# Performance work log

Measured on AMD Instinct MI355X. Metric: run time of the kernel, lower is better.

Reference implementation:

```python
import jax, jax.numpy as jnp
import numpy as np

VOCAB, EMB, HID, LAYERS, SEQ, BATCH = 10000, 1024, 1024, 2, 64, 64


def setup_inputs() -> dict:
    key = jax.random.key(0)
    ks = jax.random.split(key, 12)
    b = 1.0 / np.sqrt(HID)
    u = lambda k, shape, bd: jax.random.uniform(k, shape, jnp.float32, -bd, bd)
    return {
        "inputs": jax.random.randint(ks[0], (SEQ, BATCH), 0, VOCAB),
        "hidden": jnp.zeros((LAYERS, BATCH, HID), jnp.float32),
        "emb": u(ks[1], (VOCAB, EMB), 0.1),
        "W0": u(ks[2], (EMB, 3 * HID), b),
        "U0": u(ks[3], (HID, 3 * HID), b),
        "bw0": u(ks[4], (3 * HID,), b),
        "bu0": u(ks[5], (3 * HID,), b),
        "W1": u(ks[6], (HID, 3 * HID), b),
        "U1": u(ks[7], (HID, 3 * HID), b),
        "bw1": u(ks[8], (3 * HID,), b),
        "bu1": u(ks[9], (3 * HID,), b),
        "fcW": u(ks[10], (VOCAB, HID), 0.1),
        "fcb": jnp.zeros((VOCAB,), jnp.float32),
    }


def gru_cell(x, h, W, U, bw, bu):
    gx = x @ W + bw            # [B, 3H]
    gh = h @ U + bu            # [B, 3H]
    i_r, i_z, i_n = jnp.split(gx, 3, axis=1)
    h_r, h_z, h_n = jnp.split(gh, 3, axis=1)
    r = jax.nn.sigmoid(i_r + h_r)
    z = jax.nn.sigmoid(i_z + h_z)
    h_tilde = jnp.tanh(i_n + r * h_n)
    return (1.0 - z) * h + z * h_tilde


def reference(inputs, hidden, emb, W0, U0, bw0, bu0, W1, U1, bw1, bu1, fcW, fcb):
    # dp_keep_prob = 1.0 -> dropout is identity (eval-mode reference)
    def step(hid, tok):
        x = emb[tok]                                   # [B, EMB]
        h0 = gru_cell(x, hid[0], W0, U0, bw0, bu0)     # [B, H]
        h1 = gru_cell(h0, hid[1], W1, U1, bw1, bu1)    # [B, H]
        y = h1 @ fcW.T + fcb                           # [B, V]
        return jnp.stack([h0, h1]), y

    hidden_f, logits = jax.lax.scan(step, hidden, inputs)
    return logits, hidden_f
```

## Files before the change

### kernel.cpp

```cpp
#include <hip/hip_runtime.h>
#include <math.h>

#define SEQL 64
#define BATCHN 64
#define HID 1024
#define EMBD 1024
#define VOCAB 10000
#define G3 3072
#define NPAD 10240
#define AROWS 4096
#define HSLOT 65536

typedef float f4v __attribute__((ext_vector_type(4)));
typedef unsigned short us4 __attribute__((ext_vector_type(4)));
typedef unsigned short us8 __attribute__((ext_vector_type(8)));
typedef __bf16 bf8v __attribute__((ext_vector_type(8)));

__device__ __forceinline__ unsigned short f2bf(float f) {
    unsigned u = __float_as_uint(f);
    u += 0x7fffu + ((u >> 16) & 1u);
    return (unsigned short)(u >> 16);
}
__device__ __forceinline__ float bf2f(unsigned short h) {
    return __uint_as_float(((unsigned)h) << 16);
}
__device__ __forceinline__ void split2(float f, unsigned short &hi, unsigned short &lo) {
    hi = f2bf(f);
    lo = f2bf(f - bf2f(hi));
}
__device__ __forceinline__ f4v mfma16(us8 a, us8 b, f4v c) {
    return __builtin_amdgcn_mfma_f32_16x16x32_bf16(
        __builtin_bit_cast(bf8v, a), __builtin_bit_cast(bf8v, b), c, 0, 0, 0);
}
__device__ __forceinline__ float sigmoidf_(float x) { return 1.f / (1.f + expf(-x)); }

__device__ __forceinline__ size_t htile_off(int b, int j) {
    return ((size_t)((((b >> 4) * 32 + (j >> 5)) * 64) + ((j >> 3) & 3) * 16 + (b & 15))) * 8 + (j & 7);
}

__global__ __launch_bounds__(256)
void tile_weights_kernel(const float* __restrict__ U0, const float* __restrict__ W1,
                         const float* __restrict__ U1, const float* __restrict__ W0,
                         unsigned short* __restrict__ hi, unsigned short* __restrict__ lo)
{
    __shared__ float tile[32][65];
    const int mat = blockIdx.z;
    const float* src = (mat == 0) ? U0 : (mat == 1) ? W1 : (mat == 2) ? U1 : W0;
    const int n0 = blockIdx.x * 64, k0 = blockIdx.y * 32;
    const int t = threadIdx.x, tx = t & 63, ty = t >> 6;
#pragma unroll
    for (int s = 0; s < 8; s++)
        tile[ty * 8 + s][tx] = src[(size_t)(k0 + ty * 8 + s) * G3 + n0 + tx];
    __syncthreads();
    const int c = t >> 6, lane = t & 63, fr = lane & 15, kg = lane >> 4;
    const int cc = (n0 >> 4) + c;
    const size_t off = (((size_t)(mat * 192 + cc) * 32 + (k0 >> 5)) * 64 + lane) * 8;
    us8 h8, l8;
#pragma unroll
    for (int e = 0; e < 8; e++) {
        unsigned short a, b;
        split2(tile[kg * 8 + e][c * 16 + fr], a, b);
        h8[e] = a; l8[e] = b;
    }
    *(us8*)(hi + off) = h8;
    *(us8*)(lo + off) = l8;
}

__global__ __launch_bounds__(256)
void tile_fc_kernel(const float* __restrict__ fcW,
                    unsigned short* __restrict__ hi, unsigned short* __restrict__ lo)
{
    const int cc = blockIdx.x;
    const int tid = threadIdx.x;
#pragma unroll
    for (int q = 0; q < 8; q++) {
        const int o = tid * 8 + q;
        const int ks = o >> 6, lane = o & 63;
        const int fr = lane & 15, kg = lane >> 4;
        const int row = cc * 16 + fr;
        const int col = ks * 32 + kg * 8;
        us8 h8, l8;
        if (row < VOCAB) {
            f4v v0 = *(const f4v*)(fcW + (size_t)row * HID + col);
            f4v v1 = *(const f4v*)(fcW + (size_t)row * HID + col + 4);
#pragma unroll
            for (int e = 0; e < 4; e++) {
                unsigned short a, b;
                split2(v0[e], a, b); h8[e] = a; l8[e] = b;
                split2(v1[e], a, b); h8[4 + e] = a; l8[4 + e] = b;
            }
        } else {
            h8 = (us8){0,0,0,0,0,0,0,0};
            l8 = (us8){0,0,0,0,0,0,0,0};
        }
        const size_t off = (((size_t)cc * 32 + ks) * 64 + lane) * 8;
        *(us8*)(hi + off) = h8;
        *(us8*)(lo + off) = l8;
    }
}

__global__ void fcb_pad_kernel(const float* __restrict__ fcb, float* __restrict__ fcb_pad)
{
    int idx = blockIdx.x * 256 + threadIdx.x;
    if (idx < NPAD) fcb_pad[idx] = (idx < VOCAB) ? fcb[idx] : 0.f;
}

__global__ void small_prep_kernel(const float* __restrict__ hidden,
                                  unsigned short* __restrict__ h0th, unsigned short* __restrict__ h0tl,
                                  unsigned short* __restrict__ h1th, unsigned short* __restrict__ h1tl)
{
    int idx = blockIdx.x * 256 + threadIdx.x;
    if (idx < BATCHN * HID) {
        int b = idx >> 10, j = idx & 1023;
        size_t o = htile_off(b, j);
        unsigned short a1, b1;
        split2(hidden[idx], a1, b1);                 h0th[o] = a1; h0tl[o] = b1;
        split2(hidden[BATCHN * HID + idx], a1, b1);  h1th[o] = a1; h1tl[o] = b1;
    }
}

__global__ __launch_bounds__(256)
void gx0_gemm_kernel(const int* __restrict__ tok, const float* __restrict__ emb,
                     const unsigned short* __restrict__ Wthi, const unsigned short* __restrict__ Wtlo,
                     float* __restrict__ C)
{
    __shared__ unsigned short Ah[128][40], Al[128][40];
    const int bswz = blockIdx.x;
    const int xcd = bswz & 7, s = bswz >> 3;
    const int col0 = (xcd + 8 * (s >> 5)) * 128;
    const int row0 = (s & 31) * 128;
    const int tid = threadIdx.x;
    const int lane = tid & 63, wave = tid >> 6;
    const int wm = wave >> 1, wn = wave & 1;
    const int srow = tid >> 1;
    const int shalf = (tid & 1) * 16;

    const float* asrc = emb + (size_t)tok[row0 + srow] * EMBD + shalf;
    const int fr = lane & 15, fk = (lane >> 4) * 8;
    const int cc0 = (col0 >> 4) + wn * 4;

    f4v a[4];
#pragma unroll
    for (int q = 0; q < 4; q++) a[q] = *(const f4v*)(asrc + q * 4);

    f4v acc[4][4] = {};
    for (int k0 = 0; k0 < EMBD; k0 += 32) {
        __syncthreads();
        us8 ahv[2], alv[2];
#pragma unroll
        for (int q = 0; q < 4; q++)
#pragma unroll
            for (int j = 0; j < 4; j++) {
                unsigned short h, l;
                split2(a[q][j], h, l);
                ahv[q >> 1][(q & 1) * 4 + j] = h;
                alv[q >> 1][(q & 1) * 4 + j] = l;
            }
        *(us8*)(&Ah[srow][shalf]) = ahv[0];     *(us8*)(&Ah[srow][shalf + 8]) = ahv[1];
        *(us8*)(&Al[srow][shalf]) = alv[0];     *(us8*)(&Al[srow][shalf + 8]) = alv[1];
        __syncthreads();
        if (k0 + 32 < EMBD) {
#pragma unroll
            for (int q = 0; q < 4; q++) a[q] = *(const f4v*)(asrc + k0 + 32 + q * 4);
        }
        const int ks = k0 >> 5;
        us8 bfh[4], bfl[4];
#pragma unroll
        for (int n = 0; n < 4; n++) {
            const size_t bo = (((size_t)(3 * 192 + cc0 + n) * 32 + ks) * 64 + lane) * 8;
            bfh[n] = *(const us8*)(Wthi + bo);
            bfl[n] = *(const us8*)(Wtlo + bo);
        }
        us8 afh[4], afl[4];
#pragma unroll
        for (int m = 0; m < 4; m++) {
            afh[m] = *(const us8*)(&Ah[wm * 64 + m * 16 + fr][fk]);
            afl[m] = *(const us8*)(&Al[wm * 64 + m * 16 + fr][fk]);
        }
#pragma unroll
        for (int n = 0; n < 4; n++)
#pragma unroll
            for (int m = 0; m < 4; m++) {
                acc[m][n] = mfma16(afh[m], bfh[n], acc[m][n]);
                acc[m][n] = mfma16(afh[m], bfl[n], acc[m][n]);
                acc[m][n] = mfma16(afl[m], bfh[n], acc[m][n]);
            }
    }
    const int fq = lane >> 4;
#pragma unroll
    for (int m = 0; m < 4; m++)
#pragma unroll
        for (int n = 0; n < 4; n++)
#pragma unroll
            for (int i = 0; i < 4; i++) {
                int r = row0 + wm * 64 + m * 16 + fq * 4 + i;
                int c = col0 + wn * 64 + n * 16 + fr;
                C[(size_t)r * G3 + c] = acc[m][n][i];
            }
}

__global__ __launch_bounds__(256)
void logits_gemm_kernel(const unsigned short* __restrict__ h1t_hi, const unsigned short* __restrict__ h1t_lo,
                        const unsigned short* __restrict__ Bhi, const unsigned short* __restrict__ Blo,
                        const float* __restrict__ bias, float* __restrict__ C)
{
    const int bswz = blockIdx.x;
    const int xcd = bswz & 7, s = bswz >> 3;
    const int col0 = (xcd + 8 * (s >> 5)) * 128;
    const int row0 = (s & 31) * 128;
    const int t0 = row0 >> 6;
    const int tid = threadIdx.x;
    const int lane = tid & 63, wave = tid >> 6;
    const int wm = wave >> 1, wn = wave & 1;
    const int fr = lane & 15;
    const int cc0 = (col0 >> 4) + wn * 4;

    f4v acc[4][4] = {};
    const size_t abase = ((size_t)(t0 + wm) * 128) * 512 + (size_t)lane * 8;

    for (int ks = 0; ks < 32; ks++) {
        us8 afh[4], afl[4], bfh[4], bfl[4];
#pragma unroll
        for (int m = 0; m < 4; m++) {
            const size_t ao = abase + (size_t)(m * 32 + ks) * 512;
            afh[m] = *(const us8*)(h1t_hi + ao);
            afl[m] = *(const us8*)(h1t_lo + ao);
        }
#pragma unroll
        for (int n = 0; n < 4; n++) {
            const size_t bo = (((size_t)(cc0 + n) * 32 + ks) * 64 + lane) * 8;
            bfh[n] = *(const us8*)(Bhi + bo);
            bfl[n] = *(const us8*)(Blo + bo);
        }
#pragma unroll
        for (int n = 0; n < 4; n++)
#pragma unroll
            for (int m = 0; m < 4; m++) {
                acc[m][n] = mfma16(afh[m], bfh[n], acc[m][n]);
                acc[m][n] = mfma16(afh[m], bfl[n], acc[m][n]);
                acc[m][n] = mfma16(afl[m], bfh[n], acc[m][n]);
            }
    }
    const int fq = lane >> 4;
#pragma unroll
    for (int m = 0; m < 4; m++)
#pragma unroll
        for (int n = 0; n < 4; n++)
#pragma unroll
            for (int i = 0; i < 4; i++) {
                int r = row0 + wm * 64 + m * 16 + fq * 4 + i;
                int c = col0 + wn * 64 + n * 16 + fr;
                float v = acc[m][n][i] + bias[c];
                if (c < VOCAB) C[(size_t)r * VOCAB + c] = v;
            }
}

template <int T0, int T1>
__global__ __launch_bounds__(256)
void step_gemm_kernel(const unsigned short* __restrict__ h0hi, const unsigned short* __restrict__ h0lo,
                      const unsigned short* __restrict__ h1hi, const unsigned short* __restrict__ h1lo,
                      const unsigned short* __restrict__ Wthi, const unsigned short* __restrict__ Wtlo,
                      float* __restrict__ P)
{
    const int tid = threadIdx.x, lane = tid & 63, wave = tid >> 6;
    const int jc = blockIdx.x >> 3, kh = blockIdx.x & 7;
    const int ks = kh * 4 + wave;
    const size_t abase = ((size_t)ks * 64 + lane) * 8;

    f4v acc[9][4] = {};
    us8 ah[4], al[4];

    if (T0 < 6) {
#pragma unroll
        for (int m = 0; m < 4; m++) {
            ah[m] = *(const us8*)(h0hi + abase + (size_t)m * 16384);
            al[m] = *(const us8*)(h0lo + abase + (size_t)m * 16384);
        }
#pragma unroll
        for (int t2 = T0; t2 < ((T1 < 6) ? T1 : 6); ++t2) {
            const int mat = t2 / 3, g = t2 % 3;
            const size_t base = (((size_t)(mat * 192 + g * 64 + jc) * 32 + ks) * 64 + lane) * 8;
            us8 bh = *(const us8*)(Wthi + base);
            us8 bl = *(const us8*)(Wtlo + base);
#pragma unroll
            for (int m = 0; m < 4; ++m) {
                acc[t2][m] = mfma16(ah[m], bh, acc[t2][m]);
                acc[t2][m] = mfma16(ah[m], bl, acc[t2][m]);
                acc[t2][m] = mfma16(al[m], bh, acc[t2][m]);
            }
        }
    }
    if (T1 > 6) {
#pragma unroll
        for (int m = 0; m < 4; m++) {
            ah[m] = *(const us8*)(h1hi + abase + (size_t)m * 16384);
            al[m] = *(const us8*)(h1lo + abase + (size_t)m * 16384);
        }
#pragma unroll
        for (int t2 = 6; t2 < T1; ++t2) {
            const int g = t2 % 3;
            const size_t base = (((size_t)(2 * 192 + g * 64 + jc) * 32 + ks) * 64 + lane) * 8;
            us8 bh = *(const us8*)(Wthi + base);
            us8 bl = *(const us8*)(Wtlo + base);
#pragma unroll
            for (int m = 0; m < 4; ++m) {
                acc[t2][m] = mfma16(ah[m], bh, acc[t2][m]);
                acc[t2][m] = mfma16(ah[m], bl, acc[t2][m]);
                acc[t2][m] = mfma16(al[m], bh, acc[t2][m]);
            }
        }
    }

    __shared__ f4v red[4][2][4][64];
    const int rrow = (lane >> 4) * 4, rcol = lane & 15;
#pragma unroll
    for (int c = 0; c < 5; ++c) {
        const int ta = 2 * c, tb = 2 * c + 1;
        if (tb >= T0 && ta < T1) {
#pragma unroll
            for (int u = 0; u < 2; ++u) {
                const int t2 = 2 * c + u;
                if (t2 >= T0 && t2 < T1) {
#pragma unroll
                    for (int m = 0; m < 4; ++m)
                        red[wave][u][m][lane] = acc[t2][m];
                }
            }
            __syncthreads();
#pragma unroll
            for (int s2 = 0; s2 < 2; ++s2) {
                const int combo = wave * 2 + s2;
                const int u = combo >> 2, m = combo & 3;
                const int t2 = 2 * c + u;
                if (t2 >= T0 && t2 < T1) {
                    f4v v = (red[0][u][m][lane] + red[1][u][m][lane])
                          + (red[2][u][m][lane] + red[3][u][m][lane]);
#pragma unroll
                    for (int i = 0; i < 4; ++i)
                        P[(((size_t)kh * 9 + t2) * 64 + (m * 16 + rrow + i)) * 1024 + jc * 16 + rcol]
                            = v[i];
                }
            }
            __syncthreads();
        }
    }
}

template <int T0, int T1>
__global__ __launch_bounds__(256)
void step_reduce_kernel(const float* __restrict__ P, const float* __restrict__ gx0next,
                        const float* __restrict__ bw0, const float* __restrict__ bu0,
                        const float* __restrict__ bw1, const float* __restrict__ bu1,
                        const unsigned short* __restrict__ h0hi, const unsigned short* __restrict__ h0lo,
                        const unsigned short* __restrict__ h1hi, const unsigned short* __restrict__ h1lo,
                        unsigned short* __restrict__ h0o_hi, unsigned short* __restrict__ h0o_lo,
                        unsigned short* __restrict__ h1o_hi, unsigned short* __restrict__ h1o_lo)
{
    const int idx = blockIdx.x * 256 + threadIdx.x;
    const int b = idx >> 10, j = idx & 1023;
    float G[9];
#pragma unroll
    for (int t2 = T0; t2 < T1; t2++) {
        const float* p = P + ((size_t)t2 * 64 + b) * 1024 + j;
        float s0 = 0.f, s1 = 0.f;
#pragma unroll
        for (int kh = 0; kh < 4; kh++) {
            s0 += p[(size_t)(kh * 9) * 64 * 1024];
            s1 += p[(size_t)((kh + 4) * 9) * 64 * 1024];
        }
        G[t2] = s0 + s1;
    }
    const size_t po = htile_off(b, j);
    if (T0 == 0) {
        float sr  = gx0next[(size_t)b * G3 + j]            + bw0[j]           + G[0] + bu0[j];
        float sz  = gx0next[(size_t)b * G3 + HID + j]      + bw0[HID + j]     + G[1] + bu0[HID + j];
        float gxn = gx0next[(size_t)b * G3 + 2 * HID + j]  + bw0[2 * HID + j];
        float ghn = G[2] + bu0[2 * HID + j];
        float r = sigmoidf_(sr);
        float z = sigmoidf_(sz);
        float ht = tanhf(gxn + r * ghn);
        float hp = bf2f(h0hi[po]) + bf2f(h0lo[po]);
        float hn = (1.f - z) * hp + z * ht;
        unsigned short hh, hl2; split2(hn, hh, hl2);
        h0o_hi[po] = hh; h0o_lo[po] = hl2;
    }
    if (T1 > 3) {
        float sr  = G[3] + bw1[j]           + G[6] + bu1[j];
        float sz  = G[4] + bw1[HID + j]     + G[7] + bu1[HID + j];
        float gxn = G[5] + bw1[2 * HID + j];
        float ghn = G[8] + bu1[2 * HID + j];
        float r = sigmoidf_(sr);
        float z = sigmoidf_(sz);
        float ht = tanhf(gxn + r * ghn);
        float hp = bf2f(h1hi[po]) + bf2f(h1lo[po]);
        float hn = (1.f - z) * hp + z * ht;
        unsigned short hh, hl2; split2(hn, hh, hl2);
        h1o_hi[po] = hh; h1o_lo[po] = hl2;
    }
}

__global__ void hidden_out_kernel(const unsigned short* __restrict__ h0hi, const unsigned short* __restrict__ h0lo,
                                  const unsigned short* __restrict__ h1hi, const unsigned short* __restrict__ h1lo,
                                  float* __restrict__ out)
{
    int i = blockIdx.x * 256 + threadIdx.x;
    if (i < BATCHN * HID) {
        int b = i >> 10, j = i & 1023;
        size_t o = htile_off(b, j);
        out[i] = bf2f(h0hi[o]) + bf2f(h0lo[o]);
        out[BATCHN * HID + i] = bf2f(h1hi[o]) + bf2f(h1lo[o]);
    }
}

extern "C" void kernel_launch(void* const* d_in, const int* in_sizes, int n_in,
                              void* d_out, int out_size, void* d_ws, size_t ws_size,
                              hipStream_t stream)
{
    (void)in_sizes; (void)n_in; (void)out_size;
    const int*   tok    = (const int*)  d_in[0];
    const float* hidden = (const float*)d_in[1];
    const float* emb    = (const float*)d_in[2];
    const float* W0     = (const float*)d_in[3];
    const float* U0     = (const float*)d_in[4];
    const float* bw0    = (const float*)d_in[5];
    const float* bu0    = (const float*)d_in[6];
    const float* W1     = (const float*)d_in[7];
    const float* U1     = (const float*)d_in[8];
    const float* bw1    = (const float*)d_in[9];
    const float* bu1    = (const float*)d_in[10];
    const float* fcW    = (const float*)d_in[11];
    const float* fcb    = (const float*)d_in[12];
    float* out = (float*)d_out;

    char* wsp = (char*)d_ws;
    size_t used = 0;
    auto alloc = [&](size_t bytes) -> char* {
        char* p = wsp + used;
        used += (bytes + 255) & ~(size_t)255;
        return p;
    };
    unsigned short* Wt_hi = (unsigned short*)alloc((size_t)4 * G3 * HID * 2);
    unsigned short* Wt_lo = (unsigned short*)alloc((size_t)4 * G3 * HID * 2);
    float*          GX0   = (float*)alloc((size_t)AROWS * G3 * 4);
    unsigned short* H0Thi = (unsigned short*)alloc((size_t)SEQL * HSLOT * 2);
    unsigned short* H0Tlo = (unsigned short*)alloc((size_t)SEQL * HSLOT * 2);
    unsigned short* H1Thi = (unsigned short*)alloc((size_t)SEQL * HSLOT * 2);
    unsigned short* H1Tlo = (unsigned short*)alloc((size_t)SEQL * HSLOT * 2);
    float*          P     = (float*)alloc((size_t)8 * 9 * BATCHN * HID * 4);
    unsigned short* h0ith = (unsigned short*)alloc((size_t)HSLOT * 2);
    unsigned short* h0itl = (unsigned short*)alloc((size_t)HSLOT * 2);
    unsigned short* h1ith = (unsigned short*)alloc((size_t)HSLOT * 2);
    unsigned short* h1itl = (unsigned short*)alloc((size_t)HSLOT * 2);
    if (used > ws_size) return;

    unsigned short* fcWhi = Wt_hi;
    unsigned short* fcWlo = Wt_lo;
    float*          fcbp  = (float*)((char*)Wt_hi + (size_t)NPAD * HID * 2);

    tile_weights_kernel<<<dim3(48, 32, 4), 256, 0, stream>>>(U0, W1, U1, W0, Wt_hi, Wt_lo);
    small_prep_kernel<<<256, 256, 0, stream>>>(hidden, h0ith, h0itl, h1ith, h1itl);
    gx0_gemm_kernel<<<768, 256, 0, stream>>>(tok, emb, Wt_hi, Wt_lo, GX0);

    step_gemm_kernel<0, 3><<<512, 256, 0, stream>>>(
        h0ith, h0itl, h1ith, h1itl, Wt_hi, Wt_lo, P);
    step_reduce_kernel<0, 3><<<256, 256, 0, stream>>>(
        P, GX0, bw0, bu0, bw1, bu1,
        h0ith, h0itl, h1ith, h1itl,
        H0Thi, H0Tlo,
        H1Thi + (size_t)63 * HSLOT, H1Tlo + (size_t)63 * HSLOT);

    for (int t = 0; t < 63; t++) {
        const unsigned short* h0h = H0Thi + (size_t)t * HSLOT;
        const unsigned short* h0l = H0Tlo + (size_t)t * HSLOT;
        const unsigned short* a1h = (t == 0) ? h1ith : H1Thi + (size_t)(t - 1) * HSLOT;
        const unsigned short* a1l = (t == 0) ? h1itl : H1Tlo + (size_t)(t - 1) * HSLOT;
        step_gemm_kernel<0, 9><<<512, 256, 0, stream>>>(
            h0h, h0l, a1h, a1l, Wt_hi, Wt_lo, P);
        step_reduce_kernel<0, 9><<<256, 256, 0, stream>>>(
            P, GX0 + (size_t)(t + 1) * BATCHN * G3, bw0, bu0, bw1, bu1,
            h0h, h0l, a1h, a1l,
            H0Thi + (size_t)(t + 1) * HSLOT, H0Tlo + (size_t)(t + 1) * HSLOT,
            H1Thi + (size_t)t * HSLOT, H1Tlo + (size_t)t * HSLOT);
    }
    step_gemm_kernel<3, 9><<<512, 256, 0, stream>>>(
        H0Thi + (size_t)63 * HSLOT, H0Tlo + (size_t)63 * HSLOT,
        H1Thi + (size_t)62 * HSLOT, H1Tlo + (size_t)62 * HSLOT,
        Wt_hi, Wt_lo, P);
    step_reduce_kernel<3, 9><<<256, 256, 0, stream>>>(
        P, GX0, bw0, bu0, bw1, bu1,
        H0Thi + (size_t)63 * HSLOT, H0Tlo + (size_t)63 * HSLOT,
        H1Thi + (size_t)62 * HSLOT, H1Tlo + (size_t)62 * HSLOT,
        h0ith, h0itl,
        H1Thi + (size_t)63 * HSLOT, H1Tlo + (size_t)63 * HSLOT);

    hidden_out_kernel<<<256, 256, 0, stream>>>(
        H0Thi + (size_t)63 * HSLOT, H0Tlo + (size_t)63 * HSLOT,
        H1Thi + (size_t)63 * HSLOT, H1Tlo + (size_t)63 * HSLOT,
        out + (size_t)AROWS * VOCAB);

    tile_fc_kernel<<<NPAD / 16, 256, 0, stream>>>(fcW, fcWhi, fcWlo);
    fcb_pad_kernel<<<(NPAD + 255) / 256, 256, 0, stream>>>(fcb, fcbp);
    logits_gemm_kernel<<<2560, 256, 0, stream>>>(
        H1Thi, H1Tlo, fcWhi, fcWlo, fcbp, out);
}
```

Before: 1.555 ms.

## Stage fcW tiles in LDS for logits GEMM and fuse tail kernels

The logits GEMM now uses 512-thread blocks over 256x128 tiles. The fcW hi/lo slices are staged through padded shared memory with a register prefetch of the next k-slice, so B data is shared across more rows instead of each wave loading pre-tiled fragments from global memory. The fcW split now writes a plain row-major layout in one elementwise kernel that also pads the bias. The hidden-state output copy moves into the final step_reduce kernel. Together these remove two launches and aim to cut global B traffic, at the cost of extra barriers per k-step and shared-memory pressure.

```diff
diff --git a/kernel.cpp b/kernel.cpp
--- a/kernel.cpp
+++ b/kernel.cpp
@@ -66,43 +66,21 @@
     *(us8*)(lo + off) = l8;
 }
 
-__global__ __launch_bounds__(256)
-void tile_fc_kernel(const float* __restrict__ fcW,
-                    unsigned short* __restrict__ hi, unsigned short* __restrict__ lo)
-{
-    const int cc = blockIdx.x;
-    const int tid = threadIdx.x;
-#pragma unroll
-    for (int q = 0; q < 8; q++) {
-        const int o = tid * 8 + q;
-        const int ks = o >> 6, lane = o & 63;
-        const int fr = lane & 15, kg = lane >> 4;
-        const int row = cc * 16 + fr;
-        const int col = ks * 32 + kg * 8;
-        us8 h8, l8;
-        if (row < VOCAB) {
-            f4v v0 = *(const f4v*)(fcW + (size_t)row * HID + col);
-            f4v v1 = *(const f4v*)(fcW + (size_t)row * HID + col + 4);
-#pragma unroll
-            for (int e = 0; e < 4; e++) {
-                unsigned short a, b;
-                split2(v0[e], a, b); h8[e] = a; l8[e] = b;
-                split2(v1[e], a, b); h8[4 + e] = a; l8[4 + e] = b;
-            }
-        } else {
-            h8 = (us8){0,0,0,0,0,0,0,0};
-            l8 = (us8){0,0,0,0,0,0,0,0};
-        }
-        const size_t off = (((size_t)cc * 32 + ks) * 64 + lane) * 8;
-        *(us8*)(hi + off) = h8;
-        *(us8*)(lo + off) = l8;
-    }
-}
-
-__global__ void fcb_pad_kernel(const float* __restrict__ fcb, float* __restrict__ fcb_pad)
-{
-    int idx = blockIdx.x * 256 + threadIdx.x;
-    if (idx < NPAD) fcb_pad[idx] = (idx < VOCAB) ? fcb[idx] : 0.f;
+__global__ void fc_pad_split_kernel(const float* __restrict__ fcW,
+                                    unsigned short* __restrict__ hi, unsigned short* __restrict__ lo,
+                                    const float* __restrict__ fcb, float* __restrict__ fcb_pad)
+{
+    size_t g = (size_t)blockIdx.x * 256 + threadIdx.x;
+    if (g < NPAD) fcb_pad[g] = (g < VOCAB) ? fcb[g] : 0.f;
+    size_t i = g * 4;
+    size_t row = i >> 10;
+    f4v v = {0.f, 0.f, 0.f, 0.f};
+    if (row < VOCAB) v = *(const f4v*)(fcW + i);
+    us4 h, l;
+#pragma unroll
+    for (int j = 0; j < 4; j++) { unsigned short a, b; split2(v[j], a, b); h[j] = a; l[j] = b; }
+    *(us4*)(hi + i) = h;
+    *(us4*)(lo + i) = l;
 }
 
 __global__ void small_prep_kernel(const float* __restrict__ hidden,
@@ -199,27 +177,45 @@
             }
 }
 
-__global__ __launch_bounds__(256)
+__global__ __launch_bounds__(512)
 void logits_gemm_kernel(const unsigned short* __restrict__ h1t_hi, const unsigned short* __restrict__ h1t_lo,
                         const unsigned short* __restrict__ Bhi, const unsigned short* __restrict__ Blo,
                         const float* __restrict__ bias, float* __restrict__ C)
 {
+    __shared__ unsigned short Bh[128][40], Bl[128][40];
     const int bswz = blockIdx.x;
     const int xcd = bswz & 7, s = bswz >> 3;
-    const int col0 = (xcd + 8 * (s >> 5)) * 128;
-    const int row0 = (s & 31) * 128;
+    const int rt = xcd + 8 * (s / 80);
+    const int col0 = (s % 80) * 128;
+    const int row0 = rt * 256;
     const int t0 = row0 >> 6;
     const int tid = threadIdx.x;
     const int lane = tid & 63, wave = tid >> 6;
     const int wm = wave >> 1, wn = wave & 1;
-    const int fr = lane & 15;
-    const int cc0 = (col0 >> 4) + wn * 4;
+    const int srow = tid >> 2;
+    const int skseg = (tid & 3) * 8;
+
+    const unsigned short* bh_src = Bhi + (size_t)(col0 + srow) * HID + skseg;
+    const unsigned short* bl_src = Blo + (size_t)(col0 + srow) * HID + skseg;
 
     f4v acc[4][4] = {};
-    const size_t abase = ((size_t)(t0 + wm) * 128) * 512 + (size_t)lane * 8;
-
-    for (int ks = 0; ks < 32; ks++) {
-        us8 afh[4], afl[4], bfh[4], bfl[4];
+    us8 bh2 = *(const us8*)(bh_src);
+    us8 bl2 = *(const us8*)(bl_src);
+
+    const int fr = lane & 15, fk = (lane >> 4) * 8;
+    const size_t abase = (size_t)(t0 + wm) * HSLOT + (size_t)lane * 8;
+
+    for (int k0 = 0; k0 < HID; k0 += 32) {
+        __syncthreads();
+        *(us8*)(&Bh[srow][skseg]) = bh2;
+        *(us8*)(&Bl[srow][skseg]) = bl2;
+        __syncthreads();
+        if (k0 + 32 < HID) {
+            bh2 = *(const us8*)(bh_src + k0 + 32);
+            bl2 = *(const us8*)(bl_src + k0 + 32);
+        }
+        const int ks = k0 >> 5;
+        us8 afh[4], afl[4];
 #pragma unroll
         for (int m = 0; m < 4; m++) {
             const size_t ao = abase + (size_t)(m * 32 + ks) * 512;
@@ -228,18 +224,15 @@
         }
 #pragma unroll
         for (int n = 0; n < 4; n++) {
-            const size_t bo = (((size_t)(cc0 + n) * 32 + ks) * 64 + lane) * 8;
-            bfh[n] = *(const us8*)(Bhi + bo);
-            bfl[n] = *(const us8*)(Blo + bo);
-        }
-#pragma unroll
-        for (int n = 0; n < 4; n++)
+            us8 bfh = *(const us8*)(&Bh[wn * 64 + n * 16 + fr][fk]);
+            us8 bfl = *(const us8*)(&Bl[wn * 64 + n * 16 + fr][fk]);
 #pragma unroll
             for (int m = 0; m < 4; m++) {
-                acc[m][n] = mfma16(afh[m], bfh[n], acc[m][n]);
-                acc[m][n] = mfma16(afh[m], bfl[n], acc[m][n]);
-                acc[m][n] = mfma16(afl[m], bfh[n], acc[m][n]);
-            }
+                acc[m][n] = mfma16(afh[m], bfh, acc[m][n]);
+                acc[m][n] = mfma16(afh[m], bfl, acc[m][n]);
+                acc[m][n] = mfma16(afl[m], bfh, acc[m][n]);
+            }
+        }
     }
     const int fq = lane >> 4;
 #pragma unroll
@@ -354,7 +347,8 @@
                         const unsigned short* __restrict__ h0hi, const unsigned short* __restrict__ h0lo,
                         const unsigned short* __restrict__ h1hi, const unsigned short* __restrict__ h1lo,
                         unsigned short* __restrict__ h0o_hi, unsigned short* __restrict__ h0o_lo,
-                        unsigned short* __restrict__ h1o_hi, unsigned short* __restrict__ h1o_lo)
+                        unsigned short* __restrict__ h1o_hi, unsigned short* __restrict__ h1o_lo,
+                        float* __restrict__ outF)
 {
     const int idx = blockIdx.x * 256 + threadIdx.x;
     const int b = idx >> 10, j = idx & 1023;
@@ -396,19 +390,10 @@
         float hn = (1.f - z) * hp + z * ht;
         unsigned short hh, hl2; split2(hn, hh, hl2);
         h1o_hi[po] = hh; h1o_lo[po] = hl2;
-    }
-}
-
-__global__ void hidden_out_kernel(const unsigned short* __restrict__ h0hi, const unsigned short* __restrict__ h0lo,
-                                  const unsigned short* __restrict__ h1hi, const unsigned short* __restrict__ h1lo,
-                                  float* __restrict__ out)
-{
-    int i = blockIdx.x * 256 + threadIdx.x;
-    if (i < BATCHN * HID) {
-        int b = i >> 10, j = i & 1023;
-        size_t o = htile_off(b, j);
-        out[i] = bf2f(h0hi[o]) + bf2f(h0lo[o]);
-        out[BATCHN * HID + i] = bf2f(h1hi[o]) + bf2f(h1lo[o]);
+        if (T0 == 3) {
+            outF[(size_t)b * HID + j] = bf2f(h0hi[po]) + bf2f(h0lo[po]);
+            outF[(size_t)BATCHN * HID + b * HID + j] = hn;
+        }
     }
 }
 
@@ -457,6 +442,8 @@
     unsigned short* fcWlo = Wt_lo;
     float*          fcbp  = (float*)((char*)Wt_hi + (size_t)NPAD * HID * 2);
 
+    float* outHid = out + (size_t)AROWS * VOCAB;
+
     tile_weights_kernel<<<dim3(48, 32, 4), 256, 0, stream>>>(U0, W1, U1, W0, Wt_hi, Wt_lo);
     small_prep_kernel<<<256, 256, 0, stream>>>(hidden, h0ith, h0itl, h1ith, h1itl);
     gx0_gemm_kernel<<<768, 256, 0, stream>>>(tok, emb, Wt_hi, Wt_lo, GX0);
@@ -467,7 +454,8 @@
         P, GX0, bw0, bu0, bw1, bu1,
         h0ith, h0itl, h1ith, h1itl,
         H0Thi, H0Tlo,
-        H1Thi + (size_t)63 * HSLOT, H1Tlo + (size_t)63 * HSLOT);
+        H1Thi + (size_t)63 * HSLOT, H1Tlo + (size_t)63 * HSLOT,
+        outHid);
 
     for (int t = 0; t < 63; t++) {
         const unsigned short* h0h = H0Thi + (size_t)t * HSLOT;
@@ -480,7 +468,8 @@
             P, GX0 + (size_t)(t + 1) * BATCHN * G3, bw0, bu0, bw1, bu1,
             h0h, h0l, a1h, a1l,
             H0Thi + (size_t)(t + 1) * HSLOT, H0Tlo + (size_t)(t + 1) * HSLOT,
-            H1Thi + (size_t)t * HSLOT, H1Tlo + (size_t)t * HSLOT);
+            H1Thi + (size_t)t * HSLOT, H1Tlo + (size_t)t * HSLOT,
+            outHid);
     }
     step_gemm_kernel<3, 9><<<512, 256, 0, stream>>>(
         H0Thi + (size_t)63 * HSLOT, H0Tlo + (size_t)63 * HSLOT,
@@ -491,15 +480,10 @@
         H0Thi + (size_t)63 * HSLOT, H0Tlo + (size_t)63 * HSLOT,
         H1Thi + (size_t)62 * HSLOT, H1Tlo + (size_t)62 * HSLOT,
         h0ith, h0itl,
-        H1Thi + (size_t)63 * HSLOT, H1Tlo + (size_t)63 * HSLOT);
-
-    hidden_out_kernel<<<256, 256, 0, stream>>>(
-        H0Thi + (size_t)63 * HSLOT, H0Tlo + (size_t)63 * HSLOT,
         H1Thi + (size_t)63 * HSLOT, H1Tlo + (size_t)63 * HSLOT,
-        out + (size_t)AROWS * VOCAB);
-
-    tile_fc_kernel<<<NPAD / 16, 256, 0, stream>>>(fcW, fcWhi, fcWlo);
-    fcb_pad_kernel<<<(NPAD + 255) / 256, 256, 0, stream>>>(fcb, fcbp);
-    logits_gemm_kernel<<<2560, 256, 0, stream>>>(
+        outHid);
+
+    fc_pad_split_kernel<<<NPAD, 256, 0, stream>>>(fcW, fcWhi, fcWlo, fcb, fcbp);
+    logits_gemm_kernel<<<1280, 512, 0, stream>>>(
         H1Thi, H1Tlo, fcWhi, fcWlo, fcbp, out);
 }
```

New measurement: 1.604 ms. 1.03x slower.
